# Optimization experiments

Hardware: AMD Instinct MI355X
Metric: run time of the kernel (lower is better)

The kernel has to match this reference:

```python
import jax, jax.numpy as jnp
import numpy as np

TEMPERATURE = 0.07


def _unit(k, shape):
    x = jax.random.normal(k, shape, dtype=jnp.float32)
    return x / jnp.linalg.norm(x, axis=-1, keepdims=True)


def setup_inputs() -> dict:
    key = jax.random.key(0)
    ks = jax.random.split(key, 7)
    B, Cml, Cmc, D = 8192, 2048, 1000, 512
    features = _unit(ks[0], (B, D))
    ml_text = _unit(ks[1], (Cml, D))
    mc_text = _unit(ks[2], (Cmc, D))
    multilabel_targets = (jax.random.uniform(ks[3], (B, Cml)) < 0.05).astype(jnp.float32)
    # one-hot multiclass targets
    mc_idx = jax.random.randint(ks[4], (B,), 0, Cmc)
    multiclass_targets = jax.nn.one_hot(mc_idx, Cmc, dtype=jnp.float32)
    dataset_indices = jax.random.randint(ks[5], (B,), 0, 2).astype(jnp.int32)
    ratios = jax.random.uniform(ks[6], (Cml,), minval=0.05, maxval=0.95, dtype=jnp.float32)
    return {
        "features": features,
        "multilabel_text_features": ml_text,
        "multiclass_text_features": mc_text,
        "multilabel_targets": multilabel_targets,
        "multiclass_targets": multiclass_targets,
        "dataset_indices": dataset_indices,
        "ratios": ratios,
    }


def iterate_M(sim_matrix, b, num_iterations=2):
    # sim_matrix: [B, C, 2]; b: [C, 2]
    P = jnp.exp(sim_matrix)
    for _ in range(num_iterations):
        P = P / P.sum(axis=2, keepdims=True)          # row (last-dim) normalize
        P = P / (P.sum(axis=0) / b)                   # column normalize to marginals b
    return P


def iterate_P(sim_matrix, m, num_iterations=5):
    # sim_matrix: [B, C]
    P = jnp.exp(sim_matrix)
    for _ in range(num_iterations):
        row_sums = P.sum(axis=1)
        P = P / jnp.maximum(row_sums, 1.0)[:, None]
        P = P * m / P.sum()
    return P


def reference(features, multilabel_text_features, multiclass_text_features,
              multilabel_targets, multiclass_targets, dataset_indices, ratios):
    ml_sim = features @ multilabel_text_features.T / TEMPERATURE   # [B, Cml]
    mc_sim = features @ multiclass_text_features.T / TEMPERATURE   # [B, Cmc]

    n_mc = jnp.sum(dataset_indices == 1).astype(jnp.float32)
    n_ml = jnp.sum(dataset_indices == 0).astype(jnp.float32)
    m = n_mc + n_ml * 0.1

    P = iterate_P(mc_sim, m, 5)

    bs = ml_sim.shape[0]
    sim3 = jnp.stack([ml_sim / 2, -ml_sim / 2], axis=-1)           # [B, Cml, 2]
    b = jnp.stack([ratios, 1.0 - ratios], axis=1) * bs             # [Cml, 2]
    M = iterate_M(sim3, b, 2)

    ml_targets_final = jnp.stack([multilabel_targets, 1.0 - multilabel_targets], axis=-1)
    multilabel_loss = -jnp.sum(ml_targets_final * jnp.log(M)) * 0.5
    multiclass_loss = -jnp.sum(multiclass_targets * jnp.log(P))
    total_loss = multiclass_loss + multilabel_loss
    return total_loss
```

## Files before the change

kernel.cpp:

```cpp
#include <hip/hip_runtime.h>

typedef unsigned short u16;
typedef float f32x4 __attribute__((ext_vector_type(4)));
typedef short s16x8 __attribute__((ext_vector_type(8)));

#define GPTR(x) ((const __attribute__((address_space(1))) void*)(x))
#define LPTR(x) ((__attribute__((address_space(3))) void*)(x))

__device__ __forceinline__ u16 f32_to_bf16(float f) {
  unsigned u = __builtin_bit_cast(unsigned, f);
  u += 0x7FFFu + ((u >> 16) & 1u);
  return (u16)(u >> 16);
}
__device__ __forceinline__ float bf16_to_f32(u16 h) {
  unsigned u = ((unsigned)h) << 16;
  return __builtin_bit_cast(float, u);
}

__global__ __launch_bounds__(256) void k_cvt_all(
    const float* __restrict__ A, const float* __restrict__ ML, const float* __restrict__ MC,
    u16* __restrict__ Abf, u16* __restrict__ Bbf)
{
  int i = blockIdx.x * 256 + threadIdx.x;
  const float* src; u16* dst; int idx;
  bool pad = false;
  if (i < 1048576) { src = A; dst = Abf; idx = i; }
  else {
    int j = i - 1048576;
    if (j >= 393216) return;
    int row = j >> 7;
    dst = Bbf; idx = j;
    if (row < 2048) { src = ML; }
    else {
      int mcrow = row - 2048;
      src = MC; idx = j - 2048 * 128;
      pad = (mcrow >= 1000);
    }
  }
  ushort4 o = {0, 0, 0, 0};
  if (!pad) {
    float4 v = reinterpret_cast<const float4*>(src)[idx];
    o.x = f32_to_bf16(v.x); o.y = f32_to_bf16(v.y);
    o.z = f32_to_bf16(v.z); o.w = f32_to_bf16(v.w);
  }
  reinterpret_cast<ushort4*>(dst)[idx] = o;
}

__global__ __launch_bounds__(512) void k_gemm_fused(
    const u16* __restrict__ A, const u16* __restrict__ B,
    u16* __restrict__ Sml, float* __restrict__ colpart, float* __restrict__ pexp,
    float scale)
{
  constexpr int K = 512;
  constexpr int BK = 64;
  __shared__ __align__(16) u16 As[2][128 * BK];
  __shared__ __align__(16) u16 Bs[2][128 * BK];
  __shared__ float sred[128 * 4];

  const int tid  = threadIdx.x;
  const int lane = tid & 63;
  const int wave = tid >> 6;
  const int wr = wave >> 2;
  const int wc = wave & 3;

  int wg = (blockIdx.x & 7) * 192 + (blockIdx.x >> 3);
  const int bm = wg / 24;
  const int bn = wg % 24;
  const int row0 = bm * 128;
  const int col0 = bn * 128;
  const bool is_ml = (bn < 16);

  const int cr = (lane >> 4) * 4;
  const int cc = lane & 15;

  if (tid < 128) sred[tid] = 0.f;

  f32x4 acc[4][2];
#pragma unroll
  for (int i = 0; i < 4; ++i)
#pragma unroll
    for (int j = 0; j < 2; ++j) acc[i][j] = (f32x4){0.f, 0.f, 0.f, 0.f};

  auto stage = [&](int buf, int k0) {
#pragma unroll
    for (int q = 0; q < 2; ++q) {
      int base = wave * 128 + q * 64;
      int slot = base + lane;
      int r = slot >> 3, s = slot & 7;
      int sg = s ^ (r & 7);
      __builtin_amdgcn_global_load_lds(GPTR(A + (size_t)(row0 + r) * K + k0 + sg * 8),
                                       LPTR(&As[buf][base * 8]), 16, 0, 0);
      __builtin_amdgcn_global_load_lds(GPTR(B + (size_t)(col0 + r) * K + k0 + sg * 8),
                                       LPTR(&Bs[buf][base * 8]), 16, 0, 0);
    }
  };

  stage(0, 0);
  for (int t = 0; t < 8; ++t) {
    const int cur = t & 1;
    __syncthreads();
    if (t < 7) stage(cur ^ 1, (t + 1) * BK);
#pragma unroll
    for (int ks = 0; ks < 2; ++ks) {
      s16x8 af[4], bf[2];
#pragma unroll
      for (int mm = 0; mm < 4; ++mm) {
        int r = wr * 64 + mm * 16 + (lane & 15);
        int ss = (ks * 4 + (lane >> 4)) ^ (r & 7);
        af[mm] = *reinterpret_cast<const s16x8*>(&As[cur][r * BK + ss * 8]);
      }
#pragma unroll
      for (int nn = 0; nn < 2; ++nn) {
        int r = wc * 32 + nn * 16 + (lane & 15);
        int ss = (ks * 4 + (lane >> 4)) ^ (r & 7);
        bf[nn] = *reinterpret_cast<const s16x8*>(&Bs[cur][r * BK + ss * 8]);
      }
#pragma unroll
      for (int mm = 0; mm < 4; ++mm)
#pragma unroll
        for (int nn = 0; nn < 2; ++nn)
          acc[mm][nn] = __builtin_amdgcn_mfma_f32_16x16x32_bf16(af[mm], bf[nn], acc[mm][nn], 0, 0, 0);
    }
  }

  if (is_ml) {
#pragma unroll
    for (int mm = 0; mm < 4; ++mm) {
      int orow = row0 + wr * 64 + mm * 16 + cr;
#pragma unroll
      for (int nn = 0; nn < 2; ++nn) {
        int ocol = col0 + wc * 32 + nn * 16 + cc;
#pragma unroll
        for (int r = 0; r < 4; ++r)
          Sml[(size_t)(orow + r) * 2048 + ocol] = f32_to_bf16(acc[mm][nn][r] * scale);
      }
    }
    __syncthreads();
#pragma unroll
    for (int nn = 0; nn < 2; ++nn) {
      float cs = 0.f;
#pragma unroll
      for (int mm = 0; mm < 4; ++mm)
#pragma unroll
        for (int r = 0; r < 4; ++r) {
          float s = acc[mm][nn][r] * scale;
          cs += 1.f / (1.f + __expf(-s));
        }
      cs += __shfl_xor(cs, 16);
      cs += __shfl_xor(cs, 32);
      if (lane < 16) atomicAdd(&sred[wc * 32 + nn * 16 + lane], cs);
    }
    __syncthreads();
    if (tid < 128) colpart[(size_t)bm * 2048 + col0 + tid] = sred[tid];
  } else {
    const int mccol0 = col0 - 2048;
    float ex[16];
#pragma unroll
    for (int mm = 0; mm < 4; ++mm)
#pragma unroll
      for (int r = 0; r < 4; ++r) {
        float e = 0.f;
#pragma unroll
        for (int nn = 0; nn < 2; ++nn) {
          int ocol = mccol0 + wc * 32 + nn * 16 + cc;
          float s = acc[mm][nn][r] * scale;
          if (ocol < 1000) e += __expf(s);
        }
        ex[mm * 4 + r] = e;
      }
#pragma unroll
    for (int o = 1; o < 16; o <<= 1)
#pragma unroll
      for (int q = 0; q < 16; ++q) ex[q] += __shfl_xor(ex[q], o);
    __syncthreads();
    if ((lane & 15) == 0) {
#pragma unroll
      for (int mm = 0; mm < 4; ++mm)
#pragma unroll
        for (int r = 0; r < 4; ++r) {
          int lrow = wr * 64 + mm * 16 + cr + r;
          sred[lrow * 4 + wc] = ex[mm * 4 + r];
        }
    }
    __syncthreads();
    if (tid < 128) {
      size_t o = (size_t)(bn - 16) * 8192 + row0 + tid;
      pexp[o] = sred[tid * 4] + sred[tid * 4 + 1] + sred[tid * 4 + 2] + sred[tid * 4 + 3];
    }
  }
}

__global__ void k_reduce_c(const float* __restrict__ part, const float* __restrict__ ratios,
                           float* __restrict__ c) {
  int j = blockIdx.x * 256 + threadIdx.x;
  float s = 0.f;
  for (int ch = 0; ch < 64; ++ch) s += part[ch * 2048 + j];
  float b0 = ratios[j] * 8192.f;
  float b1 = (1.f - ratios[j]) * 8192.f;
  c[2 * j]     = b0 / s;
  c[2 * j + 1] = b1 / (8192.f - s);
}

__global__ __launch_bounds__(256) void k_ml_pass2(
    const u16* __restrict__ S, const float* __restrict__ T, const float* __restrict__ c,
    float* __restrict__ part2, float* __restrict__ partT, float* __restrict__ partE)
{
  const int t = threadIdx.x;
  const int r0 = blockIdx.x * 8;
  float c0[8], c1[8];
#pragma unroll
  for (int q = 0; q < 4; ++q) {
    float4 cv = reinterpret_cast<const float4*>(c)[t * 4 + q];
    c0[q * 2]     = cv.x; c1[q * 2]     = cv.y;
    c0[q * 2 + 1] = cv.z; c1[q * 2 + 1] = cv.w;
  }

  float q0s[8], ts[8];
#pragma unroll
  for (int k = 0; k < 8; ++k) { q0s[k] = 0.f; ts[k] = 0.f; }
  float tss = 0.f, ldsum = 0.f;

#pragma unroll 2
  for (int r = 0; r < 8; ++r) {
    size_t row = r0 + r;
    s16x8 sv = *reinterpret_cast<const s16x8*>(S + row * 2048 + t * 8);
    float4 ta = reinterpret_cast<const float4*>(T + row * 2048)[t * 2];
    float4 tb = reinterpret_cast<const float4*>(T + row * 2048)[t * 2 + 1];
    float tv[8] = {ta.x, ta.y, ta.z, ta.w, tb.x, tb.y, tb.z, tb.w};
#pragma unroll
    for (int k = 0; k < 8; ++k) {
      float s = bf16_to_f32((u16)sv[k]);
      float e = __expf(s);
      float n0 = e * c0[k];
      float den = n0 + c1[k];
      q0s[k] += n0 * __builtin_amdgcn_rcpf(den);
      ldsum  += __logf(den);
      ts[k]  += tv[k];
      tss    += tv[k] * s;
    }
  }
  float es = tss - ldsum;
#pragma unroll
  for (int k = 0; k < 8; ++k)
    es += __logf(c0[k] / c1[k]) * ts[k] + 8.f * __logf(c1[k]);

  float* p2 = part2 + (size_t)blockIdx.x * 2048 + t * 8;
  float* pT = partT + (size_t)blockIdx.x * 2048 + t * 8;
#pragma unroll
  for (int q = 0; q < 2; ++q) {
    reinterpret_cast<float4*>(p2)[q] = (float4){q0s[q*4], q0s[q*4+1], q0s[q*4+2], q0s[q*4+3]};
    reinterpret_cast<float4*>(pT)[q] = (float4){ts[q*4], ts[q*4+1], ts[q*4+2], ts[q*4+3]};
  }

  __shared__ float red[256];
  red[t] = es;
  __syncthreads();
  for (int o = 128; o; o >>= 1) {
    if (t < o) red[t] += red[t + o];
    __syncthreads();
  }
  if (t == 0) partE[blockIdx.x] = red[0];
}

__global__ __launch_bounds__(256) void k_colredA(
    const float* __restrict__ part2, const float* __restrict__ partT,
    float* __restrict__ pA2, float* __restrict__ pAT)
{
  int j = blockIdx.x * 256 + threadIdx.x;
  int ch0 = blockIdx.y * 16;
  float cs2 = 0.f, Tj = 0.f;
  for (int ch = ch0; ch < ch0 + 16; ++ch) {
    cs2 += part2[(size_t)ch * 2048 + j];
    Tj  += partT[(size_t)ch * 2048 + j];
  }
  pA2[(size_t)blockIdx.y * 2048 + j] = cs2;
  pAT[(size_t)blockIdx.y * 2048 + j] = Tj;
}

__global__ __launch_bounds__(256) void k_colredB(
    const float* __restrict__ pA2, const float* __restrict__ pAT,
    const float* __restrict__ ratios, float* __restrict__ partCol)
{
  int j = blockIdx.x * 256 + threadIdx.x;
  float cs2 = 0.f, Tj = 0.f;
  for (int ch = 0; ch < 64; ++ch) {
    cs2 += pA2[(size_t)ch * 2048 + j];
    Tj  += pAT[(size_t)ch * 2048 + j];
  }
  float b0 = ratios[j] * 8192.f;
  float b1 = (1.f - ratios[j]) * 8192.f;
  float colp = Tj * __logf(b0 / cs2) + (8192.f - Tj) * __logf(b1 / (8192.f - cs2));
  __shared__ float red[256];
  red[threadIdx.x] = colp;
  __syncthreads();
  for (int o = 128; o; o >>= 1) {
    if (threadIdx.x < o) red[threadIdx.x] += red[threadIdx.x + o];
    __syncthreads();
  }
  if (threadIdx.x == 0) partCol[blockIdx.x] = red[0];
}

__global__ __launch_bounds__(256) void k_mc_rowdot(
    const float* __restrict__ T2, const u16* __restrict__ A, const u16* __restrict__ B,
    float* __restrict__ rowdot, float scale)
{
  int wave = threadIdx.x >> 6, lane = threadIdx.x & 63;
  int row = blockIdx.x * 4 + wave;
  const float4* t4 = reinterpret_cast<const float4*>(T2 + (size_t)row * 1000);
  int idx = -1;
#pragma unroll
  for (int g = 0; g < 4; ++g) {
    int j4 = lane + g * 64;
    if (j4 < 250) {
      float4 v = t4[j4];
      if (v.x > 0.5f) idx = j4 * 4;
      if (v.y > 0.5f) idx = j4 * 4 + 1;
      if (v.z > 0.5f) idx = j4 * 4 + 2;
      if (v.w > 0.5f) idx = j4 * 4 + 3;
    }
  }
#pragma unroll
  for (int o = 32; o; o >>= 1) idx = max(idx, __shfl_xor(idx, o));

  s16x8 va = *reinterpret_cast<const s16x8*>(A + (size_t)row * 512 + lane * 8);
  s16x8 vb = *reinterpret_cast<const s16x8*>(B + (size_t)(2048 + idx) * 512 + lane * 8);
  float d = 0.f;
#pragma unroll
  for (int k = 0; k < 8; ++k)
    d += bf16_to_f32((u16)va[k]) * bf16_to_f32((u16)vb[k]);
#pragma unroll
  for (int o = 32; o; o >>= 1) d += __shfl_xor(d, o);
  if (lane == 0) rowdot[row] = d * scale;
}

__global__ __launch_bounds__(1024) void k_finalize(
    const float* __restrict__ pexp, const float* __restrict__ rowdot,
    const int* __restrict__ ds,
    const float* __restrict__ partE, const float* __restrict__ partCol,
    float* __restrict__ out)
{
  __shared__ float red[1024];
  const int tid = threadIdx.x;

  auto bsum = [&](float v) -> float {
    __syncthreads();
    red[tid] = v;
    __syncthreads();
    for (int o = 512; o; o >>= 1) {
      if (tid < o) red[tid] += red[tid + o];
      __syncthreads();
    }
    return red[0];
  };

  float nmc = 0.f, nml = 0.f;
  for (int i = tid; i < 8192; i += 1024) {
    int d = ds[i];
    nmc += (d == 1) ? 1.f : 0.f;
    nml += (d == 0) ? 1.f : 0.f;
  }
  float n_mc = bsum(nmc);
  float n_ml = bsum(nml);
  float m = n_mc + 0.1f * n_ml;

  float a[8], Rv[8], rdv[8];
#pragma unroll
  for (int q = 0; q < 8; ++q) {
    int i = tid + q * 1024;
    float e = 0.f;
#pragma unroll
    for (int ch = 0; ch < 8; ++ch) e += pexp[(size_t)ch * 8192 + i];
    Rv[q] = e; rdv[q] = rowdot[i]; a[q] = 1.f;
  }
  for (int it = 0; it < 5; ++it) {
    float p = 0.f;
#pragma unroll
    for (int q = 0; q < 8; ++q) {
      a[q] = a[q] / fmaxf(Rv[q] * a[q], 1.f);
      p += Rv[q] * a[q];
    }
    float tot = bsum(p);
    float sc = m / tot;
#pragma unroll
    for (int q = 0; q < 8; ++q) a[q] *= sc;
  }
  float mcp = 0.f;
#pragma unroll
  for (int q = 0; q < 8; ++q)
    mcp += rdv[q] + __logf(a[q]);

  float ep = partE[tid];
  float cp = 0.f;
  if (tid < 8) cp = partCol[tid];

  float total = bsum(-mcp - 0.5f * (cp + ep));
  if (tid == 0) out[0] = total;
}

extern "C" void kernel_launch(void* const* d_in, const int* in_sizes, int n_in,
                              void* d_out, int out_size, void* d_ws, size_t ws_size,
                              hipStream_t stream)
{
  const float* features = (const float*)d_in[0];
  const float* ml_text  = (const float*)d_in[1];
  const float* mc_text  = (const float*)d_in[2];
  const float* ml_tgt   = (const float*)d_in[3];
  const float* mc_tgt   = (const float*)d_in[4];
  const int*   dsidx    = (const int*)d_in[5];
  const float* ratios   = (const float*)d_in[6];
  float* out = (float*)d_out;

  char* ws = (char*)d_ws;
  size_t off = 0;
  auto alloc = [&](size_t bytes) -> void* {
    void* p = ws + off;
    off += (bytes + 255) & ~(size_t)255;
    return p;
  };
  u16*   Abf    = (u16*)alloc((size_t)8192 * 512 * 2);
  u16*   Bbf    = (u16*)alloc((size_t)3072 * 512 * 2);
  u16*   Sml    = (u16*)alloc((size_t)8192 * 2048 * 2);
  float* part1  = (float*)alloc((size_t)64 * 2048 * 4);
  float* cbuf   = (float*)alloc((size_t)2048 * 2 * 4);
  float* part2  = (float*)alloc((size_t)1024 * 2048 * 4);
  float* partT  = (float*)alloc((size_t)1024 * 2048 * 4);
  float* pA2    = (float*)alloc((size_t)64 * 2048 * 4);
  float* pAT    = (float*)alloc((size_t)64 * 2048 * 4);
  float* partE  = (float*)alloc((size_t)1024 * 4);
  float* partCol= (float*)alloc((size_t)8 * 4);
  float* pexp   = (float*)alloc((size_t)8 * 8192 * 4);
  float* rowdot = (float*)alloc((size_t)8192 * 4);

  k_cvt_all<<<(1441792 + 255) / 256, 256, 0, stream>>>(features, ml_text, mc_text, Abf, Bbf);

  const float scale = 1.0f / 0.07f;
  k_gemm_fused<<<1536, 512, 0, stream>>>(Abf, Bbf, Sml, part1, pexp, scale);

  k_mc_rowdot<<<2048, 256, 0, stream>>>(mc_tgt, Abf, Bbf, rowdot, scale);
  k_reduce_c<<<8, 256, 0, stream>>>(part1, ratios, cbuf);
  k_ml_pass2<<<1024, 256, 0, stream>>>(Sml, ml_tgt, cbuf, part2, partT, partE);
  k_colredA<<<dim3(8, 64), 256, 0, stream>>>(part2, partT, pA2, pAT);
  k_colredB<<<8, 256, 0, stream>>>(pA2, pAT, ratios, partCol);
  k_finalize<<<1, 1024, 0, stream>>>(pexp, rowdot, dsidx, partE, partCol, out);
}
```

Measured before the change: 116.5 us.

## Enlarge GEMM tile to 256x128 with triple-buffered async LDS pipeline

The fused GEMM tile grows from 128x128 to 256x128 rows per workgroup, so each wave computes 64x64 and the grid shrinks to 768 blocks. The loop now uses three LDS buffers with explicit vmcnt waits and raw s_barrier so loads run two stages ahead. MFMA issue gets a raised priority. The goal is better operand reuse and hiding global-load latency, at the cost of more registers and LDS (launch_bounds 512,1), fewer blocks for load balancing, and halved column-partial chunks.

New measurement: 122.4 us. 1.05x slower.

```diff
diff --git a/kernel.cpp b/kernel.cpp
--- a/kernel.cpp
+++ b/kernel.cpp
@@ -46,63 +46,76 @@
   reinterpret_cast<ushort4*>(dst)[idx] = o;
 }
 
-__global__ __launch_bounds__(512) void k_gemm_fused(
-    const u16* __restrict__ A, const u16* __restrict__ B,
+__global__ __launch_bounds__(512, 1) void k_gemm_fused(
+    const u16* __restrict__ A, const u16* __restrict__ Bg,
     u16* __restrict__ Sml, float* __restrict__ colpart, float* __restrict__ pexp,
     float scale)
 {
-  constexpr int K = 512;
   constexpr int BK = 64;
-  __shared__ __align__(16) u16 As[2][128 * BK];
-  __shared__ __align__(16) u16 Bs[2][128 * BK];
-  __shared__ float sred[128 * 4];
+  __shared__ __align__(16) u16 As[3][256 * BK];
+  __shared__ __align__(16) u16 Bs[3][128 * BK];
+  __shared__ float sredf[512];
 
   const int tid  = threadIdx.x;
   const int lane = tid & 63;
   const int wave = tid >> 6;
-  const int wr = wave >> 2;
-  const int wc = wave & 3;
-
-  int wg = (blockIdx.x & 7) * 192 + (blockIdx.x >> 3);
+  const int wr = wave >> 1;
+  const int wc = wave & 1;
+
+  int wg = (blockIdx.x & 7) * 96 + (blockIdx.x >> 3);
   const int bm = wg / 24;
   const int bn = wg % 24;
-  const int row0 = bm * 128;
+  const int row0 = bm * 256;
   const int col0 = bn * 128;
   const bool is_ml = (bn < 16);
 
   const int cr = (lane >> 4) * 4;
   const int cc = lane & 15;
 
-  if (tid < 128) sred[tid] = 0.f;
-
-  f32x4 acc[4][2];
+  if (tid < 128) sredf[tid] = 0.f;
+
+  f32x4 acc[4][4];
 #pragma unroll
   for (int i = 0; i < 4; ++i)
 #pragma unroll
-    for (int j = 0; j < 2; ++j) acc[i][j] = (f32x4){0.f, 0.f, 0.f, 0.f};
+    for (int j = 0; j < 4; ++j) acc[i][j] = (f32x4){0.f, 0.f, 0.f, 0.f};
 
   auto stage = [&](int buf, int k0) {
+#pragma unroll
+    for (int q = 0; q < 4; ++q) {
+      int base = wave * 256 + q * 64;
+      int slot = base + lane;
+      int r = slot >> 3, s = slot & 7;
+      int sg = s ^ (r & 7);
+      __builtin_amdgcn_global_load_lds(GPTR(A + (size_t)(row0 + r) * 512 + k0 + sg * 8),
+                                       LPTR(&As[buf][base * 8]), 16, 0, 0);
+    }
 #pragma unroll
     for (int q = 0; q < 2; ++q) {
       int base = wave * 128 + q * 64;
       int slot = base + lane;
       int r = slot >> 3, s = slot & 7;
       int sg = s ^ (r & 7);
-      __builtin_amdgcn_global_load_lds(GPTR(A + (size_t)(row0 + r) * K + k0 + sg * 8),
-                                       LPTR(&As[buf][base * 8]), 16, 0, 0);
-      __builtin_amdgcn_global_load_lds(GPTR(B + (size_t)(col0 + r) * K + k0 + sg * 8),
+      __builtin_amdgcn_global_load_lds(GPTR(Bg + (size_t)(col0 + r) * 512 + k0 + sg * 8),
                                        LPTR(&Bs[buf][base * 8]), 16, 0, 0);
     }
   };
 
   stage(0, 0);
+  stage(1, BK);
+#pragma unroll
   for (int t = 0; t < 8; ++t) {
-    const int cur = t & 1;
-    __syncthreads();
-    if (t < 7) stage(cur ^ 1, (t + 1) * BK);
+    const int cur = t % 3;
+    if (t < 7) { asm volatile("s_waitcnt vmcnt(6)" ::: "memory"); }
+    else       { asm volatile("s_waitcnt vmcnt(0)" ::: "memory"); }
+    __builtin_amdgcn_sched_barrier(0);
+    __builtin_amdgcn_s_barrier();
+    asm volatile("" ::: "memory");
+    __builtin_amdgcn_sched_barrier(0);
+    if (t + 2 < 8) stage((t + 2) % 3, (t + 2) * BK);
 #pragma unroll
     for (int ks = 0; ks < 2; ++ks) {
-      s16x8 af[4], bf[2];
+      s16x8 af[4], bf[4];
 #pragma unroll
       for (int mm = 0; mm < 4; ++mm) {
         int r = wr * 64 + mm * 16 + (lane & 15);
@@ -110,16 +123,18 @@
         af[mm] = *reinterpret_cast<const s16x8*>(&As[cur][r * BK + ss * 8]);
       }
 #pragma unroll
-      for (int nn = 0; nn < 2; ++nn) {
-        int r = wc * 32 + nn * 16 + (lane & 15);
+      for (int nn = 0; nn < 4; ++nn) {
+        int r = wc * 64 + nn * 16 + (lane & 15);
         int ss = (ks * 4 + (lane >> 4)) ^ (r & 7);
         bf[nn] = *reinterpret_cast<const s16x8*>(&Bs[cur][r * BK + ss * 8]);
       }
+      __builtin_amdgcn_s_setprio(1);
 #pragma unroll
       for (int mm = 0; mm < 4; ++mm)
 #pragma unroll
-        for (int nn = 0; nn < 2; ++nn)
+        for (int nn = 0; nn < 4; ++nn)
           acc[mm][nn] = __builtin_amdgcn_mfma_f32_16x16x32_bf16(af[mm], bf[nn], acc[mm][nn], 0, 0, 0);
+      __builtin_amdgcn_s_setprio(0);
     }
   }
 
@@ -128,16 +143,15 @@
     for (int mm = 0; mm < 4; ++mm) {
       int orow = row0 + wr * 64 + mm * 16 + cr;
 #pragma unroll
-      for (int nn = 0; nn < 2; ++nn) {
-        int ocol = col0 + wc * 32 + nn * 16 + cc;
+      for (int nn = 0; nn < 4; ++nn) {
+        int ocol = col0 + wc * 64 + nn * 16 + cc;
 #pragma unroll
         for (int r = 0; r < 4; ++r)
           Sml[(size_t)(orow + r) * 2048 + ocol] = f32_to_bf16(acc[mm][nn][r] * scale);
       }
     }
-    __syncthreads();
-#pragma unroll
-    for (int nn = 0; nn < 2; ++nn) {
+#pragma unroll
+    for (int nn = 0; nn < 4; ++nn) {
       float cs = 0.f;
 #pragma unroll
       for (int mm = 0; mm < 4; ++mm)
@@ -148,10 +162,10 @@
         }
       cs += __shfl_xor(cs, 16);
       cs += __shfl_xor(cs, 32);
-      if (lane < 16) atomicAdd(&sred[wc * 32 + nn * 16 + lane], cs);
-    }
-    __syncthreads();
-    if (tid < 128) colpart[(size_t)bm * 2048 + col0 + tid] = sred[tid];
+      if (lane < 16) atomicAdd(&sredf[wc * 64 + nn * 16 + lane], cs);
+    }
+    __syncthreads();
+    if (tid < 128) colpart[(size_t)bm * 2048 + col0 + tid] = sredf[tid];
   } else {
     const int mccol0 = col0 - 2048;
     float ex[16];
@@ -161,8 +175,8 @@
       for (int r = 0; r < 4; ++r) {
         float e = 0.f;
 #pragma unroll
-        for (int nn = 0; nn < 2; ++nn) {
-          int ocol = mccol0 + wc * 32 + nn * 16 + cc;
+        for (int nn = 0; nn < 4; ++nn) {
+          int ocol = mccol0 + wc * 64 + nn * 16 + cc;
           float s = acc[mm][nn][r] * scale;
           if (ocol < 1000) e += __expf(s);
         }
@@ -179,13 +193,13 @@
 #pragma unroll
         for (int r = 0; r < 4; ++r) {
           int lrow = wr * 64 + mm * 16 + cr + r;
-          sred[lrow * 4 + wc] = ex[mm * 4 + r];
+          sredf[lrow * 2 + wc] = ex[mm * 4 + r];
         }
     }
     __syncthreads();
-    if (tid < 128) {
+    if (tid < 256) {
       size_t o = (size_t)(bn - 16) * 8192 + row0 + tid;
-      pexp[o] = sred[tid * 4] + sred[tid * 4 + 1] + sred[tid * 4 + 2] + sred[tid * 4 + 3];
+      pexp[o] = sredf[tid * 2] + sredf[tid * 2 + 1];
     }
   }
 }
@@ -194,7 +208,7 @@
                            float* __restrict__ c) {
   int j = blockIdx.x * 256 + threadIdx.x;
   float s = 0.f;
-  for (int ch = 0; ch < 64; ++ch) s += part[ch * 2048 + j];
+  for (int ch = 0; ch < 32; ++ch) s += part[ch * 2048 + j];
   float b0 = ratios[j] * 8192.f;
   float b1 = (1.f - ratios[j]) * 8192.f;
   c[2 * j]     = b0 / s;
@@ -420,7 +434,7 @@
   u16*   Abf    = (u16*)alloc((size_t)8192 * 512 * 2);
   u16*   Bbf    = (u16*)alloc((size_t)3072 * 512 * 2);
   u16*   Sml    = (u16*)alloc((size_t)8192 * 2048 * 2);
-  float* part1  = (float*)alloc((size_t)64 * 2048 * 4);
+  float* part1  = (float*)alloc((size_t)32 * 2048 * 4);
   float* cbuf   = (float*)alloc((size_t)2048 * 2 * 4);
   float* part2  = (float*)alloc((size_t)1024 * 2048 * 4);
   float* partT  = (float*)alloc((size_t)1024 * 2048 * 4);
@@ -434,7 +448,7 @@
   k_cvt_all<<<(1441792 + 255) / 256, 256, 0, stream>>>(features, ml_text, mc_text, Abf, Bbf);
 
   const float scale = 1.0f / 0.07f;
-  k_gemm_fused<<<1536, 512, 0, stream>>>(Abf, Bbf, Sml, part1, pexp, scale);
+  k_gemm_fused<<<768, 512, 0, stream>>>(Abf, Bbf, Sml, part1, pexp, scale);
 
   k_mc_rowdot<<<2048, 256, 0, stream>>>(mc_tgt, Abf, Bbf, rowdot, scale);
   k_reduce_c<<<8, 256, 0, stream>>>(part1, ratios, cbuf);
```

## Merge small kernels, double ml_pass2 grid, fold column reduction into finalize

Applied to the files above, without the earlier changes.

Merges the c-reduction and multiclass row-dot kernels into one launch, and folds the second column-reduction stage into the single-block finalize kernel, removing two launches. ml_pass2 now handles 4 rows per block across 2048 blocks to expose more parallelism, which doubles the partial buffers and makes colredA sum 32 chunks each. The finalize block now does 64x2 column sums per thread serially, which could lengthen that single-block tail.

New measurement: 135.6 us. 16.4% more time.

```diff
diff --git a/kernel.cpp b/kernel.cpp
--- a/kernel.cpp
+++ b/kernel.cpp
@@ -190,15 +190,48 @@
   }
 }
 
-__global__ void k_reduce_c(const float* __restrict__ part, const float* __restrict__ ratios,
-                           float* __restrict__ c) {
-  int j = blockIdx.x * 256 + threadIdx.x;
-  float s = 0.f;
-  for (int ch = 0; ch < 64; ++ch) s += part[ch * 2048 + j];
-  float b0 = ratios[j] * 8192.f;
-  float b1 = (1.f - ratios[j]) * 8192.f;
-  c[2 * j]     = b0 / s;
-  c[2 * j + 1] = b1 / (8192.f - s);
+__global__ __launch_bounds__(256) void k_misc(
+    const float* __restrict__ part, const float* __restrict__ ratios, float* __restrict__ c,
+    const float* __restrict__ T2, const u16* __restrict__ A, const u16* __restrict__ B,
+    float* __restrict__ rowdot, float scale)
+{
+  if (blockIdx.x < 8) {
+    int j = blockIdx.x * 256 + threadIdx.x;
+    float s = 0.f;
+    for (int ch = 0; ch < 64; ++ch) s += part[ch * 2048 + j];
+    float b0 = ratios[j] * 8192.f;
+    float b1 = (1.f - ratios[j]) * 8192.f;
+    c[2 * j]     = b0 / s;
+    c[2 * j + 1] = b1 / (8192.f - s);
+    return;
+  }
+  int wave = threadIdx.x >> 6, lane = threadIdx.x & 63;
+  int row = (blockIdx.x - 8) * 4 + wave;
+  const float4* t4 = reinterpret_cast<const float4*>(T2 + (size_t)row * 1000);
+  int idx = -1;
+#pragma unroll
+  for (int g = 0; g < 4; ++g) {
+    int j4 = lane + g * 64;
+    if (j4 < 250) {
+      float4 v = t4[j4];
+      if (v.x > 0.5f) idx = j4 * 4;
+      if (v.y > 0.5f) idx = j4 * 4 + 1;
+      if (v.z > 0.5f) idx = j4 * 4 + 2;
+      if (v.w > 0.5f) idx = j4 * 4 + 3;
+    }
+  }
+#pragma unroll
+  for (int o = 32; o; o >>= 1) idx = max(idx, __shfl_xor(idx, o));
+
+  s16x8 va = *reinterpret_cast<const s16x8*>(A + (size_t)row * 512 + lane * 8);
+  s16x8 vb = *reinterpret_cast<const s16x8*>(B + (size_t)(2048 + idx) * 512 + lane * 8);
+  float d = 0.f;
+#pragma unroll
+  for (int k = 0; k < 8; ++k)
+    d += bf16_to_f32((u16)va[k]) * bf16_to_f32((u16)vb[k]);
+#pragma unroll
+  for (int o = 32; o; o >>= 1) d += __shfl_xor(d, o);
+  if (lane == 0) rowdot[row] = d * scale;
 }
 
 __global__ __launch_bounds__(256) void k_ml_pass2(
@@ -206,7 +239,7 @@
     float* __restrict__ part2, float* __restrict__ partT, float* __restrict__ partE)
 {
   const int t = threadIdx.x;
-  const int r0 = blockIdx.x * 8;
+  const int r0 = blockIdx.x * 4;
   float c0[8], c1[8];
 #pragma unroll
   for (int q = 0; q < 4; ++q) {
@@ -220,8 +253,8 @@
   for (int k = 0; k < 8; ++k) { q0s[k] = 0.f; ts[k] = 0.f; }
   float tss = 0.f, ldsum = 0.f;
 
-#pragma unroll 2
-  for (int r = 0; r < 8; ++r) {
+#pragma unroll
+  for (int r = 0; r < 4; ++r) {
     size_t row = r0 + r;
     s16x8 sv = *reinterpret_cast<const s16x8*>(S + row * 2048 + t * 8);
     float4 ta = reinterpret_cast<const float4*>(T + row * 2048)[t * 2];
@@ -242,7 +275,7 @@
   float es = tss - ldsum;
 #pragma unroll
   for (int k = 0; k < 8; ++k)
-    es += __logf(c0[k] / c1[k]) * ts[k] + 8.f * __logf(c1[k]);
+    es += __logf(c0[k] / c1[k]) * ts[k] + 4.f * __logf(c1[k]);
 
   float* p2 = part2 + (size_t)blockIdx.x * 2048 + t * 8;
   float* pT = partT + (size_t)blockIdx.x * 2048 + t * 8;
@@ -267,9 +300,9 @@
     float* __restrict__ pA2, float* __restrict__ pAT)
 {
   int j = blockIdx.x * 256 + threadIdx.x;
-  int ch0 = blockIdx.y * 16;
+  int ch0 = blockIdx.y * 32;
   float cs2 = 0.f, Tj = 0.f;
-  for (int ch = ch0; ch < ch0 + 16; ++ch) {
+  for (int ch = ch0; ch < ch0 + 32; ++ch) {
     cs2 += part2[(size_t)ch * 2048 + j];
     Tj  += partT[(size_t)ch * 2048 + j];
   }
@@ -277,67 +310,11 @@
   pAT[(size_t)blockIdx.y * 2048 + j] = Tj;
 }
 
-__global__ __launch_bounds__(256) void k_colredB(
-    const float* __restrict__ pA2, const float* __restrict__ pAT,
-    const float* __restrict__ ratios, float* __restrict__ partCol)
-{
-  int j = blockIdx.x * 256 + threadIdx.x;
-  float cs2 = 0.f, Tj = 0.f;
-  for (int ch = 0; ch < 64; ++ch) {
-    cs2 += pA2[(size_t)ch * 2048 + j];
-    Tj  += pAT[(size_t)ch * 2048 + j];
-  }
-  float b0 = ratios[j] * 8192.f;
-  float b1 = (1.f - ratios[j]) * 8192.f;
-  float colp = Tj * __logf(b0 / cs2) + (8192.f - Tj) * __logf(b1 / (8192.f - cs2));
-  __shared__ float red[256];
-  red[threadIdx.x] = colp;
-  __syncthreads();
-  for (int o = 128; o; o >>= 1) {
-    if (threadIdx.x < o) red[threadIdx.x] += red[threadIdx.x + o];
-    __syncthreads();
-  }
-  if (threadIdx.x == 0) partCol[blockIdx.x] = red[0];
-}
-
-__global__ __launch_bounds__(256) void k_mc_rowdot(
-    const float* __restrict__ T2, const u16* __restrict__ A, const u16* __restrict__ B,
-    float* __restrict__ rowdot, float scale)
-{
-  int wave = threadIdx.x >> 6, lane = threadIdx.x & 63;
-  int row = blockIdx.x * 4 + wave;
-  const float4* t4 = reinterpret_cast<const float4*>(T2 + (size_t)row * 1000);
-  int idx = -1;
-#pragma unroll
-  for (int g = 0; g < 4; ++g) {
-    int j4 = lane + g * 64;
-    if (j4 < 250) {
-      float4 v = t4[j4];
-      if (v.x > 0.5f) idx = j4 * 4;
-      if (v.y > 0.5f) idx = j4 * 4 + 1;
-      if (v.z > 0.5f) idx = j4 * 4 + 2;
-      if (v.w > 0.5f) idx = j4 * 4 + 3;
-    }
-  }
-#pragma unroll
-  for (int o = 32; o; o >>= 1) idx = max(idx, __shfl_xor(idx, o));
-
-  s16x8 va = *reinterpret_cast<const s16x8*>(A + (size_t)row * 512 + lane * 8);
-  s16x8 vb = *reinterpret_cast<const s16x8*>(B + (size_t)(2048 + idx) * 512 + lane * 8);
-  float d = 0.f;
-#pragma unroll
-  for (int k = 0; k < 8; ++k)
-    d += bf16_to_f32((u16)va[k]) * bf16_to_f32((u16)vb[k]);
-#pragma unroll
-  for (int o = 32; o; o >>= 1) d += __shfl_xor(d, o);
-  if (lane == 0) rowdot[row] = d * scale;
-}
-
 __global__ __launch_bounds__(1024) void k_finalize(
     const float* __restrict__ pexp, const float* __restrict__ rowdot,
-    const int* __restrict__ ds,
-    const float* __restrict__ partE, const float* __restrict__ partCol,
-    float* __restrict__ out)
+    const int* __restrict__ ds, const float* __restrict__ partE,
+    const float* __restrict__ pA2, const float* __restrict__ pAT,
+    const float* __restrict__ ratios, float* __restrict__ out)
 {
   __shared__ float red[1024];
   const int tid = threadIdx.x;
@@ -389,9 +366,21 @@
   for (int q = 0; q < 8; ++q)
     mcp += rdv[q] + __logf(a[q]);
 
-  float ep = partE[tid];
   float cp = 0.f;
-  if (tid < 8) cp = partCol[tid];
+#pragma unroll
+  for (int u = 0; u < 2; ++u) {
+    int j = tid * 2 + u;
+    float cs2 = 0.f, Tj = 0.f;
+    for (int ch = 0; ch < 64; ++ch) {
+      cs2 += pA2[(size_t)ch * 2048 + j];
+      Tj  += pAT[(size_t)ch * 2048 + j];
+    }
+    float b0 = ratios[j] * 8192.f;
+    float b1 = (1.f - ratios[j]) * 8192.f;
+    cp += Tj * __logf(b0 / cs2) + (8192.f - Tj) * __logf(b1 / (8192.f - cs2));
+  }
+
+  float ep = partE[tid] + partE[tid + 1024];
 
   float total = bsum(-mcp - 0.5f * (cp + ep));
   if (tid == 0) out[0] = total;
@@ -422,12 +411,11 @@
   u16*   Sml    = (u16*)alloc((size_t)8192 * 2048 * 2);
   float* part1  = (float*)alloc((size_t)64 * 2048 * 4);
   float* cbuf   = (float*)alloc((size_t)2048 * 2 * 4);
-  float* part2  = (float*)alloc((size_t)1024 * 2048 * 4);
-  float* partT  = (float*)alloc((size_t)1024 * 2048 * 4);
+  float* part2  = (float*)alloc((size_t)2048 * 2048 * 4);
+  float* partT  = (float*)alloc((size_t)2048 * 2048 * 4);
   float* pA2    = (float*)alloc((size_t)64 * 2048 * 4);
   float* pAT    = (float*)alloc((size_t)64 * 2048 * 4);
-  float* partE  = (float*)alloc((size_t)1024 * 4);
-  float* partCol= (float*)alloc((size_t)8 * 4);
+  float* partE  = (float*)alloc((size_t)2048 * 4);
   float* pexp   = (float*)alloc((size_t)8 * 8192 * 4);
   float* rowdot = (float*)alloc((size_t)8192 * 4);
 
@@ -436,10 +424,8 @@
   const float scale = 1.0f / 0.07f;
   k_gemm_fused<<<1536, 512, 0, stream>>>(Abf, Bbf, Sml, part1, pexp, scale);
 
-  k_mc_rowdot<<<2048, 256, 0, stream>>>(mc_tgt, Abf, Bbf, rowdot, scale);
-  k_reduce_c<<<8, 256, 0, stream>>>(part1, ratios, cbuf);
-  k_ml_pass2<<<1024, 256, 0, stream>>>(Sml, ml_tgt, cbuf, part2, partT, partE);
+  k_misc<<<8 + 2048, 256, 0, stream>>>(part1, ratios, cbuf, mc_tgt, Abf, Bbf, rowdot, scale);
+  k_ml_pass2<<<2048, 256, 0, stream>>>(Sml, ml_tgt, cbuf, part2, partT, partE);
   k_colredA<<<dim3(8, 64), 256, 0, stream>>>(part2, partT, pA2, pAT);
-  k_colredB<<<8, 256, 0, stream>>>(pA2, pAT, ratios, partCol);
-  k_finalize<<<1, 1024, 0, stream>>>(pexp, rowdot, dsidx, partE, partCol, out);
-}
+  k_finalize<<<1, 1024, 0, stream>>>(pexp, rowdot, dsidx, partE, pA2, pAT, ratios, out);
+}
```
